# Kernel tuning notes

Measured on AMD Instinct MI355X. Metric: run time of the kernel, lower is better.

The kernel has to match this reference:

```python
import jax, jax.numpy as jnp
import numpy as np

BATCH, N_DIM, N_CLASS = 32, 512, 100
BIG_NEG = 1000000.0


def _get_upper_box(z, w, b):
    # z: (B, 2, n_dim) box domain; w: (B, n_dim, S, S); b: (B, S, S)
    z_min, z_max = z[:, 0], z[:, 1]
    center = 0.5 * (z_min + z_max)      # (B, n_dim)
    radius = 0.5 * (z_max - z_min)      # (B, n_dim)
    lin = jnp.einsum('bn,bnij->bij', center, w)
    amp = jnp.einsum('bn,bnij->bij', radius, jnp.abs(w))
    return b + lin + amp


def setup_inputs() -> dict:
    key = jax.random.key(0)
    ks = jax.random.split(key, 8)
    x = jax.random.normal(ks[0], (BATCH, N_DIM), dtype=jnp.float32)
    # box domain: lower <= upper
    lower = jax.random.normal(ks[1], (BATCH, N_DIM), dtype=jnp.float32)
    width = jax.random.uniform(ks[2], (BATCH, N_DIM), dtype=jnp.float32) * 0.1
    z_tensor = jnp.stack([lower, lower + width], axis=1)  # (B, 2, n_dim)
    w_u = jax.random.normal(ks[3], (BATCH, N_DIM, N_CLASS), dtype=jnp.float32) * 0.05
    b_u = jax.random.normal(ks[4], (BATCH, N_CLASS), dtype=jnp.float32)
    w_l = jax.random.normal(ks[5], (BATCH, N_DIM, N_CLASS), dtype=jnp.float32) * 0.05
    b_l = jax.random.normal(ks[6], (BATCH, N_CLASS), dtype=jnp.float32)
    labels = jax.random.randint(ks[7], (BATCH,), 0, N_CLASS)
    y_tensor = jax.nn.one_hot(labels, N_CLASS, dtype=jnp.float32)
    return {"x": x, "z_tensor": z_tensor, "w_u": w_u, "b_u": b_u,
            "w_l": w_l, "b_l": b_l, "y_tensor": y_tensor}


def reference(x, z_tensor, w_u, b_u, w_l, b_l, y_tensor):
    # ibp=False, forward=True, mode='forward' -> adv_score = get_forward_score(...)
    source = y_tensor                 # (B, S), one-hot
    target = 1.0 - source             # (B, S)
    # broadcasted outer difference: (B, n_dim, S_target, S_source)
    w_f = w_u[:, :, :, None] - w_l[:, :, None, :]
    b_f = (b_u[:, :, None] - b_l[:, None, :]
           - BIG_NEG * (1.0 - source)[:, None, :]
           - BIG_NEG * (1.0 - target)[:, :, None])
    upper = _get_upper_box(z_tensor, w_f, b_f)  # (B, S, S)
    return jnp.max(upper, axis=(-1, -2))        # (B,)
```

## Files before the change

kernel.cpp:

```cpp
#include <hip/hip_runtime.h>
#include <math.h>
#include <stdint.h>

#define BATCH 32
#define ND 512
#define NC 100
#define NQ 8
#define BIGNEG 1000000.0f

__device__ __forceinline__ float rdlane_f(float v, int t) {
  return __uint_as_float(__builtin_amdgcn_readlane(__float_as_uint(v), (uint32_t)t));
}

__global__ __launch_bounds__(128, 8) void adv_part(
    const float* __restrict__ z, const float* __restrict__ wu,
    const float* __restrict__ wl, const float* __restrict__ y,
    float* __restrict__ P)
{
  const int id = ((blockIdx.x & 7) << 5) + (blockIdx.x >> 3);
  const int b = id >> 3, nq = id & 7;
  const int tid  = threadIdx.x;
  const int half = tid >> 6, l = tid & 63;

  __shared__ int   s_js;
  __shared__ float s_dq;

  if (tid == 0) s_js = 0;
  __syncthreads();
  if (tid < NC && y[b * NC + tid] > 0.5f) s_js = tid;
  __syncthreads();
  const int js = s_js;

  const int n0 = nq << 6;
  const int n  = n0 + l;
  const float* zb = z + (size_t)b * 2 * ND;
  const float zlo = zb[n], zhi = zb[ND + n];
  const float cc = zlo + zhi;
  const float rr = zhi - zlo;
  const float qv = wl[((size_t)b * ND + n) * NC + js];

  if (half == 0) {
    float p = cc * qv;
#pragma unroll
    for (int off = 1; off < 64; off <<= 1) p += __shfl_xor(p, off, 64);
    if (l == 0) s_dq = p;
  }

  const int i  = (half << 6) + l;
  const int iL = (i < NC) ? i : NC - 1;
  const float* up = wu + ((size_t)b * ND + n0) * NC + iL;

  float amp = 0.f, dotu = 0.f;
#pragma unroll 16
  for (int t = 0; t < 64; ++t) {
    float u  = up[(size_t)t * NC];
    float cs = rdlane_f(cc, t);
    float rs = rdlane_f(rr, t);
    float qs = rdlane_f(qv, t);
    float d  = u - qs;
    amp  = fmaf(rs, fabsf(d), amp);
    dotu = fmaf(cs, u, dotu);
  }
  __syncthreads();
  P[(size_t)id * 128 + tid] = amp + dotu - s_dq;
}

__global__ __launch_bounds__(128) void adv_fin(
    const float* __restrict__ P, const float* __restrict__ bu,
    const float* __restrict__ bl, const float* __restrict__ y,
    float* __restrict__ out)
{
  const int b = blockIdx.x, tid = threadIdx.x;
  __shared__ int   s_js;
  __shared__ float s_mx[2];

  if (tid == 0) s_js = 0;
  __syncthreads();
  if (tid < NC && y[b * NC + tid] > 0.5f) s_js = tid;
  __syncthreads();
  const int js = s_js;

  float m = -INFINITY;
  if (tid < NC) {
    const float* pb = P + ((size_t)b * NQ) * 128 + tid;
    float s = 0.f;
#pragma unroll
    for (int q = 0; q < NQ; ++q) s += pb[q * 128];
    m = bu[b * NC + tid] - BIGNEG * y[b * NC + tid] - bl[b * NC + js] + 0.5f * s;
  }
#pragma unroll
  for (int off = 32; off; off >>= 1) m = fmaxf(m, __shfl_down(m, off, 64));
  if ((tid & 63) == 0) s_mx[tid >> 6] = m;
  __syncthreads();
  if (tid == 0) out[b] = fmaxf(s_mx[0], s_mx[1]);
}

extern "C" void kernel_launch(void* const* d_in, const int* in_sizes, int n_in,
                              void* d_out, int out_size, void* d_ws, size_t ws_size,
                              hipStream_t stream) {
  const float* z  = (const float*)d_in[1];
  const float* wu = (const float*)d_in[2];
  const float* bu = (const float*)d_in[3];
  const float* wl = (const float*)d_in[4];
  const float* bl = (const float*)d_in[5];
  const float* y  = (const float*)d_in[6];
  float* P = (float*)d_ws;

  adv_part<<<BATCH * NQ, 128, 0, stream>>>(z, wu, wl, y, P);
  adv_fin<<<BATCH, 128, 0, stream>>>(P, bu, bl, y, (float*)d_out);
}
```

Measured before the change: 11.77 us.

## Fuse partial and final kernels via last-block atomic counter, split n across waves

Merges the two-kernel partial-sum plus finalize pipeline into a single kernel, where the last block per batch (found with an atomic counter and threadfence) does the final reduction and max. Each block now uses 256 threads, and the two n-halves are summed through shared memory, which shortens each wave's serial loop from 64 to 32 iterations. This removes one kernel launch gap and raises the wave count per block. In exchange it adds a hipMemsetAsync on every call, plus atomics and fence overhead.

New measurement: 28.07 us. 2.38x slower.

```diff
diff --git a/kernel.cpp b/kernel.cpp
--- a/kernel.cpp
+++ b/kernel.cpp
@@ -5,73 +5,27 @@
 #define BATCH 32
 #define ND 512
 #define NC 100
-#define NQ 8
 #define BIGNEG 1000000.0f
 
 __device__ __forceinline__ float rdlane_f(float v, int t) {
   return __uint_as_float(__builtin_amdgcn_readlane(__float_as_uint(v), (uint32_t)t));
 }
 
-__global__ __launch_bounds__(128, 8) void adv_part(
+__global__ __launch_bounds__(256, 8) void adv_all(
     const float* __restrict__ z, const float* __restrict__ wu,
-    const float* __restrict__ wl, const float* __restrict__ y,
-    float* __restrict__ P)
+    const float* __restrict__ wl, const float* __restrict__ bu,
+    const float* __restrict__ bl, const float* __restrict__ y,
+    float* __restrict__ P, int* __restrict__ cnt, float* __restrict__ out)
 {
   const int id = ((blockIdx.x & 7) << 5) + (blockIdx.x >> 3);
   const int b = id >> 3, nq = id & 7;
-  const int tid  = threadIdx.x;
-  const int half = tid >> 6, l = tid & 63;
+  const int tid = threadIdx.x;
+  const int wv = tid >> 6, l = tid & 63;
+  const int ns = wv & 1, ih = wv >> 1;
 
-  __shared__ int   s_js;
-  __shared__ float s_dq;
-
-  if (tid == 0) s_js = 0;
-  __syncthreads();
-  if (tid < NC && y[b * NC + tid] > 0.5f) s_js = tid;
-  __syncthreads();
-  const int js = s_js;
-
-  const int n0 = nq << 6;
-  const int n  = n0 + l;
-  const float* zb = z + (size_t)b * 2 * ND;
-  const float zlo = zb[n], zhi = zb[ND + n];
-  const float cc = zlo + zhi;
-  const float rr = zhi - zlo;
-  const float qv = wl[((size_t)b * ND + n) * NC + js];
-
-  if (half == 0) {
-    float p = cc * qv;
-#pragma unroll
-    for (int off = 1; off < 64; off <<= 1) p += __shfl_xor(p, off, 64);
-    if (l == 0) s_dq = p;
-  }
-
-  const int i  = (half << 6) + l;
-  const int iL = (i < NC) ? i : NC - 1;
-  const float* up = wu + ((size_t)b * ND + n0) * NC + iL;
-
-  float amp = 0.f, dotu = 0.f;
-#pragma unroll 16
-  for (int t = 0; t < 64; ++t) {
-    float u  = up[(size_t)t * NC];
-    float cs = rdlane_f(cc, t);
-    float rs = rdlane_f(rr, t);
-    float qs = rdlane_f(qv, t);
-    float d  = u - qs;
-    amp  = fmaf(rs, fabsf(d), amp);
-    dotu = fmaf(cs, u, dotu);
-  }
-  __syncthreads();
-  P[(size_t)id * 128 + tid] = amp + dotu - s_dq;
-}
-
-__global__ __launch_bounds__(128) void adv_fin(
-    const float* __restrict__ P, const float* __restrict__ bu,
-    const float* __restrict__ bl, const float* __restrict__ y,
-    float* __restrict__ out)
-{
-  const int b = blockIdx.x, tid = threadIdx.x;
-  __shared__ int   s_js;
+  __shared__ int s_js, s_last;
+  __shared__ float s_dq[2];
+  __shared__ float s_p[128];
   __shared__ float s_mx[2];
 
   if (tid == 0) s_js = 0;
@@ -80,19 +34,65 @@
   __syncthreads();
   const int js = s_js;
 
+  const int n0 = (nq << 6) + (ns << 5);
+  const int nl = n0 + (l & 31);
+  const float* zb = z + (size_t)b * 2 * ND;
+  const float zlo = zb[nl], zhi = zb[ND + nl];
+  const float cc = zlo + zhi;
+  const float rr = zhi - zlo;
+  const float qv = wl[((size_t)b * ND + nl) * NC + js];
+
+  if (ih == 0) {
+    float p = cc * qv;
+#pragma unroll
+    for (int off = 1; off < 32; off <<= 1) p += __shfl_xor(p, off, 64);
+    if (l == 0) s_dq[ns] = p;
+  }
+
+  const int i  = (ih << 6) + l;
+  const int iL = (i < NC) ? i : NC - 1;
+  const float* up = wu + ((size_t)b * ND + n0) * NC + iL;
+
+  float amp = 0.f, dot = 0.f;
+#pragma unroll
+  for (int t = 0; t < 32; ++t) {
+    float u  = up[(size_t)t * NC];
+    float cs = rdlane_f(cc, t);
+    float rs = rdlane_f(rr, t);
+    float qs = rdlane_f(qv, t);
+    float d  = u - qs;
+    amp = fmaf(rs, fabsf(d), amp);
+    dot = fmaf(cs, u, dot);
+  }
+  const float v = amp + dot;
+  if (ns == 1) s_p[i] = v;
+  __syncthreads();
+  if (ns == 0)
+    P[(size_t)id * 128 + i] = v + s_p[i] - (s_dq[0] + s_dq[1]);
+  __threadfence();
+  __syncthreads();
+  if (tid == 0) s_last = (atomicAdd(&cnt[b], 1) == 7);
+  __syncthreads();
+  if (!s_last) return;
+
   float m = -INFINITY;
-  if (tid < NC) {
-    const float* pb = P + ((size_t)b * NQ) * 128 + tid;
+  if (tid < 128) {
+    const float* pb = P + ((size_t)(b << 3)) * 128 + tid;
     float s = 0.f;
 #pragma unroll
-    for (int q = 0; q < NQ; ++q) s += pb[q * 128];
-    m = bu[b * NC + tid] - BIGNEG * y[b * NC + tid] - bl[b * NC + js] + 0.5f * s;
+    for (int q = 0; q < 8; ++q)
+      s += __hip_atomic_load(pb + (q << 7), __ATOMIC_RELAXED, __HIP_MEMORY_SCOPE_AGENT);
+    if (tid < NC)
+      m = bu[b * NC + tid] - BIGNEG * y[b * NC + tid] - bl[b * NC + js] + 0.5f * s;
   }
 #pragma unroll
   for (int off = 32; off; off >>= 1) m = fmaxf(m, __shfl_down(m, off, 64));
-  if ((tid & 63) == 0) s_mx[tid >> 6] = m;
+  if (tid < 128 && (tid & 63) == 0) s_mx[tid >> 6] = m;
   __syncthreads();
-  if (tid == 0) out[b] = fmaxf(s_mx[0], s_mx[1]);
+  if (tid == 0) {
+    out[b] = fmaxf(s_mx[0], s_mx[1]);
+    cnt[b] = 0;
+  }
 }
 
 extern "C" void kernel_launch(void* const* d_in, const int* in_sizes, int n_in,
@@ -104,8 +104,10 @@
   const float* wl = (const float*)d_in[4];
   const float* bl = (const float*)d_in[5];
   const float* y  = (const float*)d_in[6];
-  float* P = (float*)d_ws;
 
-  adv_part<<<BATCH * NQ, 128, 0, stream>>>(z, wu, wl, y, P);
-  adv_fin<<<BATCH, 128, 0, stream>>>(P, bu, bl, y, (float*)d_out);
+  int*   cnt = (int*)d_ws;
+  float* P   = (float*)((char*)d_ws + 512);
+
+  hipMemsetAsync(cnt, 0, BATCH * sizeof(int), stream);
+  adv_all<<<BATCH * 8, 256, 0, stream>>>(z, wu, wl, bu, bl, y, P, cnt, (float*)d_out);
 }
```
